# Kernel optimization log

Hardware: AMD Instinct MI355X
Metric: run time of the kernel (lower is better)

## Reference

```python
import jax, jax.numpy as jnp
import numpy as np
from jax import lax

IN, H1, H2, OUT = 256, 512, 512, 1
T, B = 2048, 64


def lstm_layer(x, W_ih, W_hh, b_ih, b_hh):
    # x: (T, B, I); W_ih: (4H, I); W_hh: (4H, H); biases: (4H,)
    H = W_hh.shape[1]
    # precompute input contribution for all timesteps (one big GEMM)
    xg = jnp.einsum('tbi,gi->tbg', x, W_ih) + b_ih + b_hh  # (T, B, 4H)

    def step(carry, xg_t):
        h, c = carry
        gates = xg_t + h @ W_hh.T  # (B, 4H), PyTorch gate order i,f,g,o
        i, f, g, o = jnp.split(gates, 4, axis=-1)
        c = jax.nn.sigmoid(f) * c + jax.nn.sigmoid(i) * jnp.tanh(g)
        h = jax.nn.sigmoid(o) * jnp.tanh(c)
        return (h, c), h

    h0 = jnp.zeros((x.shape[1], H), x.dtype)
    _, hs = lax.scan(step, (h0, h0), xg)
    return hs  # (T, B, H)


def setup_inputs() -> dict:
    key = jax.random.key(0)
    ks = jax.random.split(key, 11)
    s1 = 1.0 / np.sqrt(H1)
    s2 = 1.0 / np.sqrt(H2)
    inp = {
        'input': jax.random.normal(ks[0], (T, B, IN), jnp.float32),
        'W_ih1': jax.random.uniform(ks[1], (4 * H1, IN), jnp.float32, -s1, s1),
        'W_hh1': jax.random.uniform(ks[2], (4 * H1, H1), jnp.float32, -s1, s1),
        'b_ih1': jax.random.uniform(ks[3], (4 * H1,), jnp.float32, -s1, s1),
        'b_hh1': jax.random.uniform(ks[4], (4 * H1,), jnp.float32, -s1, s1),
        'W_ih2': jax.random.uniform(ks[5], (4 * H2, H1), jnp.float32, -s2, s2),
        'W_hh2': jax.random.uniform(ks[6], (4 * H2, H2), jnp.float32, -s2, s2),
        'b_ih2': jax.random.uniform(ks[7], (4 * H2,), jnp.float32, -s2, s2),
        'b_hh2': jax.random.uniform(ks[8], (4 * H2,), jnp.float32, -s2, s2),
        'W_out': jax.random.uniform(ks[9], (OUT, H2), jnp.float32, -s2, s2),
        'b_out': jax.random.uniform(ks[10], (OUT,), jnp.float32, -s2, s2),
    }
    return inp


def reference(input, W_ih1, W_hh1, b_ih1, b_hh1, W_ih2, W_hh2, b_ih2, b_hh2, W_out, b_out):
    h1 = lstm_layer(input, W_ih1, W_hh1, b_ih1, b_hh1)   # (T, B, H1)
    h2 = lstm_layer(h1, W_ih2, W_hh2, b_ih2, b_hh2)      # (T, B, H2)
    out = jnp.einsum('tbh,oh->tbo', h2, W_out) + b_out   # (T, B, OUT)
    return jax.nn.sigmoid(out)
```

## Files before the change

### kernel.cpp

```cpp
#include <hip/hip_runtime.h>
#include <math.h>

#define T_STEPS 2048
#define BATCH   64
#define HDIM    512
#define GDIM    2048
#define INDIM   256
#define NBLK_RE 128
#define HB_STEP (HDIM * BATCH)

typedef _Float16 f16x8 __attribute__((ext_vector_type(8)));
typedef _Float16 f16x4 __attribute__((ext_vector_type(4)));
typedef float    f32x4 __attribute__((ext_vector_type(4)));

__device__ __forceinline__ float sigf(float x) { return 1.0f / (1.0f + __expf(-x)); }
__device__ __forceinline__ float tanh_fast(float x) {
    return 1.0f - 2.0f / (__expf(2.0f * x) + 1.0f);
}

__global__ __launch_bounds__(256) void cvt_f16(const float* __restrict__ src,
                                               _Float16* __restrict__ dst, int n4)
{
    int i = blockIdx.x * 256 + threadIdx.x;
    if (i < n4) {
        float4 v = ((const float4*)src)[i];
        f16x4 h;
        h[0] = (_Float16)v.x; h[1] = (_Float16)v.y;
        h[2] = (_Float16)v.z; h[3] = (_Float16)v.w;
        ((f16x4*)dst)[i] = h;
    }
}

__device__ __forceinline__ void wait_flags_wave(const unsigned* __restrict__ flags,
                                                unsigned tgt, int ln)
{
    const unsigned* p0 = flags + (size_t)ln * 16;
    const unsigned* p1 = flags + (size_t)(ln + 64) * 16;
    for (;;) {
        unsigned f0 = __hip_atomic_load(p0, __ATOMIC_RELAXED, __HIP_MEMORY_SCOPE_AGENT);
        unsigned f1 = __hip_atomic_load(p1, __ATOMIC_RELAXED, __HIP_MEMORY_SCOPE_AGENT);
        if (__all((int)(f0 >= tgt) & (int)(f1 >= tgt))) break;
    }
    __atomic_signal_fence(__ATOMIC_ACQUIRE);
}

__global__ __launch_bounds__(256, 1) void lstm_fused(
    const _Float16* __restrict__ xh,
    const _Float16* __restrict__ Wf1h,
    const _Float16* __restrict__ Wf1i,
    const _Float16* __restrict__ Wf2i,
    const _Float16* __restrict__ Wf2h,
    const float* __restrict__ bih1, const float* __restrict__ bhh1,
    const float* __restrict__ bih2, const float* __restrict__ bhh2,
    _Float16* __restrict__ hb1,
    _Float16* __restrict__ hb2,
    float* __restrict__ c1,
    float* __restrict__ c2,
    unsigned* __restrict__ flag1,
    unsigned* __restrict__ flag2,
    int nsteps, unsigned t0a)
{
    __shared__ float    gl[16][68];
    __shared__ _Float16 hsm[64][4];

    const int tid   = threadIdx.x;
    const int layer = blockIdx.x >> 7;
    const int wg    = blockIdx.x & (NBLK_RE - 1);
    const int j0    = wg * 4;
    const int wv    = tid >> 6;
    const int ln    = tid & 63;
    const int l16   = ln & 15;
    const int quad  = ln >> 4;
    const int grow  = (l16 >> 2) * HDIM + j0 + (l16 & 3);
    const int du    = wv;
    const int bu    = tid & 63;
    const int dd    = j0 + du;

    if (layer == 0) {
        f16x8 Bh[16], Bx[8];
#pragma unroll
        for (int j = 0; j < 16; j++) {
            const uint4 u = *(const uint4*)&Wf1h[(size_t)grow * HDIM + j * 32 + quad * 8];
            Bh[j] = __builtin_bit_cast(f16x8, u);
        }
#pragma unroll
        for (int j = 0; j < 8; j++) {
            const uint4 u = *(const uint4*)&Wf1i[(size_t)grow * INDIM + j * 32 + quad * 8];
            Bx[j] = __builtin_bit_cast(f16x8, u);
        }
        float c_reg = c1[(size_t)dd * BATCH + bu];
        const float bi_ = bih1[0 * HDIM + dd] + bhh1[0 * HDIM + dd];
        const float bf_ = bih1[1 * HDIM + dd] + bhh1[1 * HDIM + dd];
        const float bg_ = bih1[2 * HDIM + dd] + bhh1[2 * HDIM + dd];
        const float bo_ = bih1[3 * HDIM + dd] + bhh1[3 * HDIM + dd];

        for (int t = 0; t < nsteps; t++) {
            f32x4 ax0 = {0.f, 0.f, 0.f, 0.f}, ax1 = {0.f, 0.f, 0.f, 0.f};

            {
                const _Float16* xp = xh + ((size_t)t * BATCH + 16 * wv + l16) * INDIM
                                   + quad * 8;
                ulonglong2 ax[8];
#pragma unroll
                for (int j = 0; j < 8; j++)
                    ax[j] = *(const ulonglong2*)(xp + j * 32);
#pragma unroll
                for (int j = 0; j < 8; j += 2) {
                    ax0 = __builtin_amdgcn_mfma_f32_16x16x32_f16(
                        __builtin_bit_cast(f16x8, ax[j]),     Bx[j],     ax0, 0, 0, 0);
                    ax1 = __builtin_amdgcn_mfma_f32_16x16x32_f16(
                        __builtin_bit_cast(f16x8, ax[j + 1]), Bx[j + 1], ax1, 0, 0, 0);
                }
            }

            wait_flags_wave(flag1, t0a + (unsigned)t, ln);
            f32x4 ah0 = {0.f, 0.f, 0.f, 0.f}, ah1 = {0.f, 0.f, 0.f, 0.f};
            f32x4 ah2 = {0.f, 0.f, 0.f, 0.f}, ah3 = {0.f, 0.f, 0.f, 0.f};
            {
                const _Float16* hp = hb1 + (size_t)t * HB_STEP
                                   + (size_t)(16 * wv + l16) * HDIM + quad * 8;
                ulonglong2 a[16];
#pragma unroll
                for (int j = 0; j < 16; j++)
                    a[j] = *(const ulonglong2*)(hp + j * 32);
#pragma unroll
                for (int j = 0; j < 16; j += 4) {
                    ah0 = __builtin_amdgcn_mfma_f32_16x16x32_f16(
                        __builtin_bit_cast(f16x8, a[j]),     Bh[j],     ah0, 0, 0, 0);
                    ah1 = __builtin_amdgcn_mfma_f32_16x16x32_f16(
                        __builtin_bit_cast(f16x8, a[j + 1]), Bh[j + 1], ah1, 0, 0, 0);
                    ah2 = __builtin_amdgcn_mfma_f32_16x16x32_f16(
                        __builtin_bit_cast(f16x8, a[j + 2]), Bh[j + 2], ah2, 0, 0, 0);
                    ah3 = __builtin_amdgcn_mfma_f32_16x16x32_f16(
                        __builtin_bit_cast(f16x8, a[j + 3]), Bh[j + 3], ah3, 0, 0, 0);
                }
            }
            f32x4 d = (ax0 + ax1) + ((ah0 + ah1) + (ah2 + ah3));
            *(f32x4*)&gl[l16][16 * wv + quad * 4] = d;
            __syncthreads();

            {
                float si = gl[4 * 0 + du][bu] + bi_;
                float sf = gl[4 * 1 + du][bu] + bf_;
                float sg = gl[4 * 2 + du][bu] + bg_;
                float so = gl[4 * 3 + du][bu] + bo_;
                c_reg = sigf(sf) * c_reg + sigf(si) * tanh_fast(sg);
                float h = sigf(so) * tanh_fast(c_reg);
                hsm[bu][du] = (_Float16)h;
            }
            __syncthreads();

            if (tid < 64) {
                unsigned long long pk = *(const unsigned long long*)&hsm[tid][0];
                unsigned long long* dst = (unsigned long long*)
                    (hb1 + (size_t)(t + 1) * HB_STEP + (size_t)tid * HDIM + j0);
                __hip_atomic_store(dst, pk, __ATOMIC_RELAXED, __HIP_MEMORY_SCOPE_AGENT);
                if (t == nsteps - 1) {
                    unsigned long long* dst0 = (unsigned long long*)
                        (hb1 + (size_t)tid * HDIM + j0);
                    __hip_atomic_store(dst0, pk, __ATOMIC_RELAXED, __HIP_MEMORY_SCOPE_AGENT);
                }
                if (tid == 0) {
                    asm volatile("s_waitcnt vmcnt(0)" ::: "memory");
                    __hip_atomic_store(flag1 + (size_t)wg * 16, t0a + (unsigned)t + 1u,
                                       __ATOMIC_RELAXED, __HIP_MEMORY_SCOPE_AGENT);
                }
            }
        }
        c1[(size_t)dd * BATCH + bu] = c_reg;
    } else {
        f16x8 Bh[16], Bi[16];
#pragma unroll
        for (int j = 0; j < 16; j++) {
            const uint4 uh = *(const uint4*)&Wf2h[(size_t)grow * HDIM + j * 32 + quad * 8];
            Bh[j] = __builtin_bit_cast(f16x8, uh);
            const uint4 ui = *(const uint4*)&Wf2i[(size_t)grow * HDIM + j * 32 + quad * 8];
            Bi[j] = __builtin_bit_cast(f16x8, ui);
        }
        float c_reg = c2[(size_t)dd * BATCH + bu];
        const float bi_ = bih2[0 * HDIM + dd] + bhh2[0 * HDIM + dd];
        const float bf_ = bih2[1 * HDIM + dd] + bhh2[1 * HDIM + dd];
        const float bg_ = bih2[2 * HDIM + dd] + bhh2[2 * HDIM + dd];
        const float bo_ = bih2[3 * HDIM + dd] + bhh2[3 * HDIM + dd];

        for (int t = 0; t < nsteps; t++) {
            f32x4 ai0 = {0.f, 0.f, 0.f, 0.f}, ai1 = {0.f, 0.f, 0.f, 0.f};
            f32x4 ag0 = {0.f, 0.f, 0.f, 0.f}, ag1 = {0.f, 0.f, 0.f, 0.f};

            wait_flags_wave(flag1, t0a + (unsigned)t + 1u, ln);
            {
                const _Float16* hp = hb1 + (size_t)(t + 1) * HB_STEP
                                   + (size_t)(16 * wv + l16) * HDIM + quad * 8;
                ulonglong2 a[16];
#pragma unroll
                for (int j = 0; j < 16; j++)
                    a[j] = *(const ulonglong2*)(hp + j * 32);
#pragma unroll
                for (int j = 0; j < 16; j += 2) {
                    ai0 = __builtin_amdgcn_mfma_f32_16x16x32_f16(
                        __builtin_bit_cast(f16x8, a[j]),     Bi[j],     ai0, 0, 0, 0);
                    ai1 = __builtin_amdgcn_mfma_f32_16x16x32_f16(
                        __builtin_bit_cast(f16x8, a[j + 1]), Bi[j + 1], ai1, 0, 0, 0);
                }
            }

            wait_flags_wave(flag2, t0a + (unsigned)t, ln);
            {
                const _Float16* hp = hb2 + (size_t)t * HB_STEP
                                   + (size_t)(16 * wv + l16) * HDIM + quad * 8;
                ulonglong2 a[16];
#pragma unroll
                for (int j = 0; j < 16; j++)
                    a[j] = *(const ulonglong2*)(hp + j * 32);
#pragma unroll
                for (int j = 0; j < 16; j += 2) {
                    ag0 = __builtin_amdgcn_mfma_f32_16x16x32_f16(
                        __builtin_bit_cast(f16x8, a[j]),     Bh[j],     ag0, 0, 0, 0);
                    ag1 = __builtin_amdgcn_mfma_f32_16x16x32_f16(
                        __builtin_bit_cast(f16x8, a[j + 1]), Bh[j + 1], ag1, 0, 0, 0);
                }
            }
            f32x4 d = (ai0 + ai1) + (ag0 + ag1);
            *(f32x4*)&gl[l16][16 * wv + quad * 4] = d;
            __syncthreads();

            {
                float si = gl[4 * 0 + du][bu] + bi_;
                float sf = gl[4 * 1 + du][bu] + bf_;
                float sg = gl[4 * 2 + du][bu] + bg_;
                float so = gl[4 * 3 + du][bu] + bo_;
                c_reg = sigf(sf) * c_reg + sigf(si) * tanh_fast(sg);
                float h = sigf(so) * tanh_fast(c_reg);
                hsm[bu][du] = (_Float16)h;
            }
            __syncthreads();

            if (tid < 64) {
                unsigned long long pk = *(const unsigned long long*)&hsm[tid][0];
                unsigned long long* dst = (unsigned long long*)
                    (hb2 + (size_t)(t + 1) * HB_STEP + (size_t)tid * HDIM + j0);
                __hip_atomic_store(dst, pk, __ATOMIC_RELAXED, __HIP_MEMORY_SCOPE_AGENT);
                if (t == nsteps - 1) {
                    unsigned long long* dst0 = (unsigned long long*)
                        (hb2 + (size_t)tid * HDIM + j0);
                    __hip_atomic_store(dst0, pk, __ATOMIC_RELAXED, __HIP_MEMORY_SCOPE_AGENT);
                }
                if (tid == 0) {
                    asm volatile("s_waitcnt vmcnt(0)" ::: "memory");
                    __hip_atomic_store(flag2 + (size_t)wg * 16, t0a + (unsigned)t + 1u,
                                       __ATOMIC_RELAXED, __HIP_MEMORY_SCOPE_AGENT);
                }
            }
        }
        c2[(size_t)dd * BATCH + bu] = c_reg;
    }
}

__global__ __launch_bounds__(256) void out_kernel(
    const _Float16* __restrict__ h2, const float* __restrict__ Wout,
    const float* __restrict__ bout, float* __restrict__ out)
{
    const int t = blockIdx.x;
    const int q = threadIdx.x >> 6, b = threadIdx.x & 63;
    const _Float16* base = &h2[(size_t)t * HB_STEP + (size_t)b * HDIM];
    float s = 0.0f;
#pragma unroll 8
    for (int k = q * 128; k < q * 128 + 128; k += 4) {
        const uint2 u = *(const uint2*)&base[k];
        f16x4 h = __builtin_bit_cast(f16x4, u);
        s += Wout[k] * (float)h[0] + Wout[k + 1] * (float)h[1]
           + Wout[k + 2] * (float)h[2] + Wout[k + 3] * (float)h[3];
    }
    __shared__ float red[4][64];
    red[q][b] = s;
    __syncthreads();
    if (q == 0) {
        float v = red[0][b] + red[1][b] + red[2][b] + red[3][b] + bout[0];
        out[t * BATCH + b] = sigf(v);
    }
}

static size_t req_bytes(int C) {
    return 65536
         + 2ull * HDIM * BATCH * 4
         + 3ull * GDIM * HDIM * 2
         + (size_t)GDIM * INDIM * 2
         + (size_t)T_STEPS * BATCH * INDIM * 2
         + 2ull * (size_t)(C + 1) * BATCH * HDIM * 2;
}

extern "C" void kernel_launch(void* const* d_in, const int* in_sizes, int n_in,
                              void* d_out, int out_size, void* d_ws, size_t ws_size,
                              hipStream_t stream)
{
    const float* x    = (const float*)d_in[0];
    const float* Wih1 = (const float*)d_in[1];
    const float* Whh1 = (const float*)d_in[2];
    const float* bih1 = (const float*)d_in[3];
    const float* bhh1 = (const float*)d_in[4];
    const float* Wih2 = (const float*)d_in[5];
    const float* Whh2 = (const float*)d_in[6];
    const float* bih2 = (const float*)d_in[7];
    const float* bhh2 = (const float*)d_in[8];
    const float* Wout = (const float*)d_in[9];
    const float* bout = (const float*)d_in[10];
    float* out = (float*)d_out;

    int C = 8;
    const int cands[] = {2048, 1024, 512, 256, 128, 64, 32, 16, 8};
    for (int i = 0; i < 9; i++)
        if (req_bytes(cands[i]) <= ws_size) { C = cands[i]; break; }

    char* p = (char*)d_ws;
    unsigned*  flag1 = (unsigned*)p;                p += 32768;
    unsigned*  flag2 = (unsigned*)p;                p += 32768;
    float*     c1    = (float*)p;                   p += (size_t)HDIM * BATCH * 4;
    float*     c2    = (float*)p;                   p += (size_t)HDIM * BATCH * 4;
    _Float16*  Wf1h  = (_Float16*)p;                p += (size_t)GDIM * HDIM * 2;
    _Float16*  Wf1i  = (_Float16*)p;                p += (size_t)GDIM * INDIM * 2;
    _Float16*  Wf2i  = (_Float16*)p;                p += (size_t)GDIM * HDIM * 2;
    _Float16*  Wf2h  = (_Float16*)p;                p += (size_t)GDIM * HDIM * 2;
    _Float16*  xh    = (_Float16*)p;                p += (size_t)T_STEPS * BATCH * INDIM * 2;
    _Float16*  hb1   = (_Float16*)p;                p += (size_t)(C + 1) * BATCH * HDIM * 2;
    _Float16*  hb2   = (_Float16*)p;

    hipMemsetAsync(flag1, 0, 65536 + 2ull * HDIM * BATCH * 4, stream);
    hipMemsetAsync(hb1, 0, (size_t)BATCH * HDIM * 2, stream);
    hipMemsetAsync(hb2, 0, (size_t)BATCH * HDIM * 2, stream);

    cvt_f16<<<dim3(GDIM * HDIM / 4 / 256), dim3(256), 0, stream>>>(Whh1, Wf1h, GDIM * HDIM / 4);
    cvt_f16<<<dim3(GDIM * INDIM / 4 / 256), dim3(256), 0, stream>>>(Wih1, Wf1i, GDIM * INDIM / 4);
    cvt_f16<<<dim3(GDIM * HDIM / 4 / 256), dim3(256), 0, stream>>>(Wih2, Wf2i, GDIM * HDIM / 4);
    cvt_f16<<<dim3(GDIM * HDIM / 4 / 256), dim3(256), 0, stream>>>(Whh2, Wf2h, GDIM * HDIM / 4);
    cvt_f16<<<dim3(T_STEPS * BATCH * INDIM / 4 / 256), dim3(256), 0, stream>>>(
        x, xh, T_STEPS * BATCH * INDIM / 4);

    const _Float16* h2r = hb2 + (size_t)HB_STEP;

    for (int t0 = 0; t0 < T_STEPS; t0 += C) {
        const _Float16* xc = xh + (size_t)t0 * BATCH * INDIM;
        unsigned t0a = (unsigned)t0;
        void* args[] = {(void*)&xc, (void*)&Wf1h, (void*)&Wf1i, (void*)&Wf2i,
                        (void*)&Wf2h, (void*)&bih1, (void*)&bhh1, (void*)&bih2,
                        (void*)&bhh2, (void*)&hb1, (void*)&hb2, (void*)&c1,
                        (void*)&c2, (void*)&flag1, (void*)&flag2, (void*)&C,
                        (void*)&t0a};
        hipLaunchCooperativeKernel((void*)lstm_fused, dim3(2 * NBLK_RE), dim3(256),
                                   args, 0, stream);

        out_kernel<<<dim3(C), dim3(256), 0, stream>>>(h2r, Wout, bout,
                                                      out + (size_t)t0 * BATCH);
    }

    (void)in_sizes; (void)n_in; (void)out_size;
}
```

Measured before the change: 12.59 ms.

## Partition recurrent work into four independent batch groups with group-local flag sync

Each workgroup now owns 16 hidden units for a 16-row batch slice, instead of 4 hidden units for the full batch. The 128 workgroups per layer form 4 independent batch groups of 32. Each workgroup waits only on the 32 flags of its own group, since its batch rows depend only on h from those rows. This shrinks the cross-workgroup dependency fan-in and the flag polling per step. The cost is a changed LDS layout and smaller per-workgroup MFMA M dimension, and the weight rows per workgroup change.

```diff
diff --git a/kernel.cpp b/kernel.cpp
--- a/kernel.cpp
+++ b/kernel.cpp
@@ -8,6 +8,9 @@
 #define INDIM   256
 #define NBLK_RE 128
 #define HB_STEP (HDIM * BATCH)
+#define GROUPS  4
+#define WPG     32
+#define BPG     16
 
 typedef _Float16 f16x8 __attribute__((ext_vector_type(8)));
 typedef _Float16 f16x4 __attribute__((ext_vector_type(4)));
@@ -31,15 +34,15 @@
     }
 }
 
-__device__ __forceinline__ void wait_flags_wave(const unsigned* __restrict__ flags,
-                                                unsigned tgt, int ln)
-{
-    const unsigned* p0 = flags + (size_t)ln * 16;
-    const unsigned* p1 = flags + (size_t)(ln + 64) * 16;
+__device__ __forceinline__ void wait_flags_grp(const unsigned* __restrict__ flags,
+                                               int g, unsigned tgt, int ln)
+{
+    const unsigned* p = flags + (size_t)(g * WPG + (ln & 31)) * 16;
     for (;;) {
-        unsigned f0 = __hip_atomic_load(p0, __ATOMIC_RELAXED, __HIP_MEMORY_SCOPE_AGENT);
-        unsigned f1 = __hip_atomic_load(p1, __ATOMIC_RELAXED, __HIP_MEMORY_SCOPE_AGENT);
-        if (__all((int)(f0 >= tgt) & (int)(f1 >= tgt))) break;
+        unsigned f = (ln < 32)
+            ? __hip_atomic_load(p, __ATOMIC_RELAXED, __HIP_MEMORY_SCOPE_AGENT)
+            : tgt;
+        if (__all((int)(f >= tgt))) break;
     }
     __atomic_signal_fence(__ATOMIC_ACQUIRE);
 }
@@ -60,21 +63,25 @@
     unsigned* __restrict__ flag2,
     int nsteps, unsigned t0a)
 {
-    __shared__ float    gl[16][68];
-    __shared__ _Float16 hsm[64][4];
+    __shared__ float    gl[4][16][20];
+    __shared__ _Float16 hsm[16][16];
 
     const int tid   = threadIdx.x;
     const int layer = blockIdx.x >> 7;
-    const int wg    = blockIdx.x & (NBLK_RE - 1);
-    const int j0    = wg * 4;
+    const int wgl   = blockIdx.x & (NBLK_RE - 1);
+    const int g     = wgl >> 5;
+    const int w     = wgl & 31;
+    const int j0    = w * 16;
     const int wv    = tid >> 6;
     const int ln    = tid & 63;
     const int l16   = ln & 15;
     const int quad  = ln >> 4;
-    const int grow  = (l16 >> 2) * HDIM + j0 + (l16 & 3);
-    const int du    = wv;
-    const int bu    = tid & 63;
-    const int dd    = j0 + du;
+    const int grow  = (l16 >> 2) * HDIM + j0 + 4 * wv + (l16 & 3);
+    const int d16   = tid >> 4;
+    const int b16   = tid & 15;
+    const int dd    = j0 + d16;
+    const int bu    = g * BPG + b16;
+    const int arow  = g * BPG + l16;
 
     if (layer == 0) {
         f16x8 Bh[16], Bx[8];
@@ -98,7 +105,7 @@
             f32x4 ax0 = {0.f, 0.f, 0.f, 0.f}, ax1 = {0.f, 0.f, 0.f, 0.f};
 
             {
-                const _Float16* xp = xh + ((size_t)t * BATCH + 16 * wv + l16) * INDIM
+                const _Float16* xp = xh + ((size_t)t * BATCH + arow) * INDIM
                                    + quad * 8;
                 ulonglong2 ax[8];
 #pragma unroll
@@ -113,12 +120,12 @@
                 }
             }
 
-            wait_flags_wave(flag1, t0a + (unsigned)t, ln);
+            wait_flags_grp(flag1, g, t0a + (unsigned)t, ln);
             f32x4 ah0 = {0.f, 0.f, 0.f, 0.f}, ah1 = {0.f, 0.f, 0.f, 0.f};
             f32x4 ah2 = {0.f, 0.f, 0.f, 0.f}, ah3 = {0.f, 0.f, 0.f, 0.f};
             {
                 const _Float16* hp = hb1 + (size_t)t * HB_STEP
-                                   + (size_t)(16 * wv + l16) * HDIM + quad * 8;
+                                   + (size_t)arow * HDIM + quad * 8;
                 ulonglong2 a[16];
 #pragma unroll
                 for (int j = 0; j < 16; j++)
@@ -136,33 +143,35 @@
                 }
             }
             f32x4 d = (ax0 + ax1) + ((ah0 + ah1) + (ah2 + ah3));
-            *(f32x4*)&gl[l16][16 * wv + quad * 4] = d;
+            *(f32x4*)&gl[l16 >> 2][4 * wv + (l16 & 3)][quad * 4] = d;
             __syncthreads();
 
             {
-                float si = gl[4 * 0 + du][bu] + bi_;
-                float sf = gl[4 * 1 + du][bu] + bf_;
-                float sg = gl[4 * 2 + du][bu] + bg_;
-                float so = gl[4 * 3 + du][bu] + bo_;
+                float si = gl[0][d16][b16] + bi_;
+                float sf = gl[1][d16][b16] + bf_;
+                float sg = gl[2][d16][b16] + bg_;
+                float so = gl[3][d16][b16] + bo_;
                 c_reg = sigf(sf) * c_reg + sigf(si) * tanh_fast(sg);
                 float h = sigf(so) * tanh_fast(c_reg);
-                hsm[bu][du] = (_Float16)h;
+                hsm[b16][d16] = (_Float16)h;
             }
             __syncthreads();
 
             if (tid < 64) {
-                unsigned long long pk = *(const unsigned long long*)&hsm[tid][0];
+                const int pb = tid >> 2, pd = tid & 3;
+                unsigned long long pk = *(const unsigned long long*)&hsm[pb][pd * 4];
                 unsigned long long* dst = (unsigned long long*)
-                    (hb1 + (size_t)(t + 1) * HB_STEP + (size_t)tid * HDIM + j0);
+                    (hb1 + (size_t)(t + 1) * HB_STEP
+                         + (size_t)(g * BPG + pb) * HDIM + j0 + pd * 4);
                 __hip_atomic_store(dst, pk, __ATOMIC_RELAXED, __HIP_MEMORY_SCOPE_AGENT);
                 if (t == nsteps - 1) {
                     unsigned long long* dst0 = (unsigned long long*)
-                        (hb1 + (size_t)tid * HDIM + j0);
+                        (hb1 + (size_t)(g * BPG + pb) * HDIM + j0 + pd * 4);
                     __hip_atomic_store(dst0, pk, __ATOMIC_RELAXED, __HIP_MEMORY_SCOPE_AGENT);
                 }
                 if (tid == 0) {
                     asm volatile("s_waitcnt vmcnt(0)" ::: "memory");
-                    __hip_atomic_store(flag1 + (size_t)wg * 16, t0a + (unsigned)t + 1u,
+                    __hip_atomic_store(flag1 + (size_t)wgl * 16, t0a + (unsigned)t + 1u,
                                        __ATOMIC_RELAXED, __HIP_MEMORY_SCOPE_AGENT);
                 }
             }
@@ -187,10 +196,10 @@
             f32x4 ai0 = {0.f, 0.f, 0.f, 0.f}, ai1 = {0.f, 0.f, 0.f, 0.f};
             f32x4 ag0 = {0.f, 0.f, 0.f, 0.f}, ag1 = {0.f, 0.f, 0.f, 0.f};
 
-            wait_flags_wave(flag1, t0a + (unsigned)t + 1u, ln);
+            wait_flags_grp(flag1, g, t0a + (unsigned)t + 1u, ln);
             {
                 const _Float16* hp = hb1 + (size_t)(t + 1) * HB_STEP
-                                   + (size_t)(16 * wv + l16) * HDIM + quad * 8;
+                                   + (size_t)arow * HDIM + quad * 8;
                 ulonglong2 a[16];
 #pragma unroll
                 for (int j = 0; j < 16; j++)
@@ -204,10 +213,10 @@
                 }
             }
 
-            wait_flags_wave(flag2, t0a + (unsigned)t, ln);
+            wait_flags_grp(flag2, g, t0a + (unsigned)t, ln);
             {
                 const _Float16* hp = hb2 + (size_t)t * HB_STEP
-                                   + (size_t)(16 * wv + l16) * HDIM + quad * 8;
+                                   + (size_t)arow * HDIM + quad * 8;
                 ulonglong2 a[16];
 #pragma unroll
                 for (int j = 0; j < 16; j++)
@@ -221,33 +230,35 @@
                 }
             }
             f32x4 d = (ai0 + ai1) + (ag0 + ag1);
-            *(f32x4*)&gl[l16][16 * wv + quad * 4] = d;
+            *(f32x4*)&gl[l16 >> 2][4 * wv + (l16 & 3)][quad * 4] = d;
             __syncthreads();
 
             {
-                float si = gl[4 * 0 + du][bu] + bi_;
-                float sf = gl[4 * 1 + du][bu] + bf_;
-                float sg = gl[4 * 2 + du][bu] + bg_;
-                float so = gl[4 * 3 + du][bu] + bo_;
+                float si = gl[0][d16][b16] + bi_;
+                float sf = gl[1][d16][b16] + bf_;
+                float sg = gl[2][d16][b16] + bg_;
+                float so = gl[3][d16][b16] + bo_;
                 c_reg = sigf(sf) * c_reg + sigf(si) * tanh_fast(sg);
                 float h = sigf(so) * tanh_fast(c_reg);
-                hsm[bu][du] = (_Float16)h;
+                hsm[b16][d16] = (_Float16)h;
             }
             __syncthreads();
 
             if (tid < 64) {
-                unsigned long long pk = *(const unsigned long long*)&hsm[tid][0];
+                const int pb = tid >> 2, pd = tid & 3;
+                unsigned long long pk = *(const unsigned long long*)&hsm[pb][pd * 4];
                 unsigned long long* dst = (unsigned long long*)
-                    (hb2 + (size_t)(t + 1) * HB_STEP + (size_t)tid * HDIM + j0);
+                    (hb2 + (size_t)(t + 1) * HB_STEP
+                         + (size_t)(g * BPG + pb) * HDIM + j0 + pd * 4);
                 __hip_atomic_store(dst, pk, __ATOMIC_RELAXED, __HIP_MEMORY_SCOPE_AGENT);
                 if (t == nsteps - 1) {
                     unsigned long long* dst0 = (unsigned long long*)
-                        (hb2 + (size_t)tid * HDIM + j0);
+                        (hb2 + (size_t)(g * BPG + pb) * HDIM + j0 + pd * 4);
                     __hip_atomic_store(dst0, pk, __ATOMIC_RELAXED, __HIP_MEMORY_SCOPE_AGENT);
                 }
                 if (tid == 0) {
                     asm volatile("s_waitcnt vmcnt(0)" ::: "memory");
-                    __hip_atomic_store(flag2 + (size_t)wg * 16, t0a + (unsigned)t + 1u,
+                    __hip_atomic_store(flag2 + (size_t)wgl * 16, t0a + (unsigned)t + 1u,
                                        __ATOMIC_RELAXED, __HIP_MEMORY_SCOPE_AGENT);
                 }
             }
```

Result: faster. 11.43 ms, median of 2 (-9.2%).
